# Performance work log

Hardware: AMD Instinct MI355X
Metric: run time of the kernel (lower is better)

Reference implementation:

```python
import jax, jax.numpy as jnp
import numpy as np

# Model dims
B, T, D = 1, 2048, 2048          # batch, seq_len, d_model
HI, DI = 4, 64                   # indexer heads / dim
H, DH = 16, 128                  # attention heads / head dim (H*DH == D)
TOPK = 512                       # sparse top-k tokens per query
NEG = -1e9


def setup_inputs() -> dict:
    key = jax.random.key(0)
    ks = jax.random.split(key, 8)
    s = 0.02  # weight init scale
    return {
        "hidden_states": jax.random.normal(ks[0], (B, T, D), jnp.float32),
        "Wq_idx": jax.random.normal(ks[1], (D, HI * DI), jnp.float32) * s,
        "Wk_idx": jax.random.normal(ks[2], (D, DI), jnp.float32) * s,
        "Ww_idx": jax.random.normal(ks[3], (D, HI), jnp.float32) * s,
        "Wq": jax.random.normal(ks[4], (D, H * DH), jnp.float32) * s,
        "Wk": jax.random.normal(ks[5], (D, H * DH), jnp.float32) * s,
        "Wv": jax.random.normal(ks[6], (D, H * DH), jnp.float32) * s,
        "Wo": jax.random.normal(ks[7], (H * DH, D), jnp.float32) * s,
    }


def reference(hidden_states, Wq_idx, Wk_idx, Ww_idx, Wq, Wk, Wv, Wo):
    x = hidden_states
    # ---- Lightning indexer: I[t,s] = sum_j w[t,j] * relu(q[t,j] . k[s]) ----
    qi = (x @ Wq_idx).reshape(B, T, HI, DI)          # [B,T,HI,DI]
    ki = x @ Wk_idx                                   # [B,S,DI]
    w = x @ Ww_idx                                    # [B,T,HI]
    dots = jnp.einsum('bthd,bsd->bths', qi, ki)       # [B,T,HI,S]
    index_scores = (jax.nn.relu(dots) * w[..., None]).sum(axis=2)  # [B,T,S]

    # ---- Top-k token selection with causal mask ----
    causal = jnp.triu(jnp.ones((T, T), dtype=bool), 1)            # True above diag
    masked_scores = jnp.where(causal[None], NEG, index_scores)
    _, top_idx = jax.lax.top_k(masked_scores, TOPK)               # [B,T,TOPK]
    b_ix = jnp.arange(B)[:, None, None]
    t_ix = jnp.arange(T)[None, :, None]
    top_mask = jnp.zeros((B, T, T), dtype=bool).at[b_ix, t_ix, top_idx].set(True)
    add_mask = jnp.where(top_mask, 0.0, NEG).astype(x.dtype)      # [B,T,S]

    # ---- Dense multi-head attention with additive sparse mask ----
    q = (x @ Wq).reshape(B, T, H, DH)
    k = (x @ Wk).reshape(B, T, H, DH)
    v = (x @ Wv).reshape(B, T, H, DH)
    scores = jnp.einsum('bthd,bshd->bhts', q, k) / np.sqrt(DH).astype(np.float32)
    scores = scores + add_mask[:, None]                            # [B,H,T,S]
    probs = jax.nn.softmax(scores, axis=-1)
    attn = jnp.einsum('bhts,bshd->bthd', probs, v).reshape(B, T, H * DH)
    attn_output = attn @ Wo                                        # [B,T,D]
    return attn_output
```

## Files before the change

kernel.cpp:

```cpp
#include <hip/hip_runtime.h>
#include <cstdint>
#include <cstddef>

#define T_DIM 2048
#define D_DIM 2048
#define HI_N 4
#define DI_N 64
#define H_N 16
#define DH_N 128
#define TOPK_N 512
#define NEG_F (-1e9f)
#define FA_NEG (-1e30f)

typedef __attribute__((ext_vector_type(8))) short short8;
typedef __attribute__((ext_vector_type(4))) float f32x4;
typedef unsigned short ushort_t;

__device__ __forceinline__ unsigned short f2bf(float f) {
  unsigned u = __float_as_uint(f);
  u += 0x7FFFu + ((u >> 16) & 1u);
  return (unsigned short)(u >> 16);
}
__device__ __forceinline__ float bf2f(unsigned short b) {
  return __uint_as_float((unsigned)b << 16);
}

#define GLDS(g, l) __builtin_amdgcn_global_load_lds( \
    (const __attribute__((address_space(1))) unsigned int*)(g), \
    (__attribute__((address_space(3))) unsigned int*)(l), 16, 0, 0)

#define IDXP_QI_F   524288
#define IDXP_KI_F   131072
#define IDXP_WI_F   8192
#define IDXP_STRIDE (IDXP_QI_F + IDXP_KI_F + IDXP_WI_F)

__global__ __launch_bounds__(256) void idx_proj(const float* __restrict__ x,
                                                const float* __restrict__ Wq_idx,
                                                const float* __restrict__ Wk_idx,
                                                const float* __restrict__ Ww_idx,
                                                float* __restrict__ parts) {
  __shared__ float As[2][16][64];
  __shared__ float Bs[2][16][64];
  const int bm = blockIdx.y << 6;
  const int bn_id = blockIdx.x;
  const int kbeg = blockIdx.z << 9;
  const int kend = kbeg + 512;
  float* part = parts + (size_t)blockIdx.z * IDXP_STRIDE;
  const float* B; float* C; int ldB, cb, ncols;
  if (bn_id < 4)       { B = Wq_idx; C = part;             ldB = 256; cb = bn_id << 6; ncols = 64; }
  else if (bn_id == 4) { B = Wk_idx; C = part + IDXP_QI_F; ldB = 64;  cb = 0;          ncols = 64; }
  else                 { B = Ww_idx; C = part + IDXP_QI_F + IDXP_KI_F; ldB = 4; cb = 0; ncols = 4; }
  const int tid = threadIdx.x;
  const int tx = tid & 15, ty = tid >> 4;
  const int am = tid >> 2;
  const int ak = (tid & 3) << 2;
  float acc[4][4] = {};

  float4 a4 = *(const float4*)&x[(size_t)(bm + am) * 2048 + kbeg + ak];
  float4 b4 = make_float4(0, 0, 0, 0);
  if ((tx << 2) < ncols) b4 = *(const float4*)&B[(size_t)(kbeg + ty) * ldB + cb + (tx << 2)];
  As[0][ak + 0][am] = a4.x; As[0][ak + 1][am] = a4.y;
  As[0][ak + 2][am] = a4.z; As[0][ak + 3][am] = a4.w;
  *(float4*)&Bs[0][ty][tx << 2] = b4;

  int p = 0;
  for (int k0 = kbeg; k0 < kend; k0 += 16) {
    __syncthreads();
    const bool more = (k0 + 16) < kend;
    if (more) {
      a4 = *(const float4*)&x[(size_t)(bm + am) * 2048 + k0 + 16 + ak];
      if ((tx << 2) < ncols)
        b4 = *(const float4*)&B[(size_t)(k0 + 16 + ty) * ldB + cb + (tx << 2)];
    }
#pragma unroll
    for (int kk = 0; kk < 16; ++kk) {
      float4 av4 = *(const float4*)&As[p][kk][ty << 2];
      float4 bv4 = *(const float4*)&Bs[p][kk][tx << 2];
      float av[4] = {av4.x, av4.y, av4.z, av4.w};
      float bv[4] = {bv4.x, bv4.y, bv4.z, bv4.w};
#pragma unroll
      for (int i = 0; i < 4; ++i)
#pragma unroll
        for (int j = 0; j < 4; ++j) acc[i][j] += av[i] * bv[j];
    }
    if (more) {
      As[1 - p][ak + 0][am] = a4.x; As[1 - p][ak + 1][am] = a4.y;
      As[1 - p][ak + 2][am] = a4.z; As[1 - p][ak + 3][am] = a4.w;
      *(float4*)&Bs[1 - p][ty][tx << 2] = b4;
    }
    p ^= 1;
  }
#pragma unroll
  for (int i = 0; i < 4; ++i) {
    int m = bm + (ty << 2) + i;
    int n0 = tx << 2;
    if (n0 + 3 < ncols) {
      *(float4*)&C[(size_t)m * ldB + cb + n0] =
          make_float4(acc[i][0], acc[i][1], acc[i][2], acc[i][3]);
    } else {
#pragma unroll
      for (int j = 0; j < 4; ++j)
        if (n0 + j < ncols) C[(size_t)m * ldB + cb + n0 + j] = acc[i][j];
    }
  }
}

__global__ __launch_bounds__(256) void idx_reduce(const float* __restrict__ parts,
                                                  float* __restrict__ qi,
                                                  float* __restrict__ ki,
                                                  float* __restrict__ wI) {
  const size_t f = ((size_t)blockIdx.x * 256 + threadIdx.x) * 4;
  float4 r0 = *(const float4*)(parts + f);
  float4 r1 = *(const float4*)(parts + (size_t)IDXP_STRIDE + f);
  float4 r2 = *(const float4*)(parts + (size_t)2 * IDXP_STRIDE + f);
  float4 r3 = *(const float4*)(parts + (size_t)3 * IDXP_STRIDE + f);
  float4 r;
  r.x = ((r0.x + r1.x) + r2.x) + r3.x;
  r.y = ((r0.y + r1.y) + r2.y) + r3.y;
  r.z = ((r0.z + r1.z) + r2.z) + r3.z;
  r.w = ((r0.w + r1.w) + r2.w) + r3.w;
  float* dst;
  if (f < IDXP_QI_F)                     dst = qi + f;
  else if (f < IDXP_QI_F + IDXP_KI_F)    dst = ki + (f - IDXP_QI_F);
  else                                   dst = wI + (f - IDXP_QI_F - IDXP_KI_F);
  *(float4*)dst = r;
}

__global__ __launch_bounds__(256) void cast_bf16(const float* __restrict__ in,
                                                 ushort_t* __restrict__ out) {
  int i = (blockIdx.x * 256 + threadIdx.x) * 4;
  float4 f = *(const float4*)(in + i);
  ushort4 o;
  o.x = f2bf(f.x); o.y = f2bf(f.y); o.z = f2bf(f.z); o.w = f2bf(f.w);
  *(ushort4*)(out + i) = o;
}

__global__ __launch_bounds__(256) void cast_transpose(const float* __restrict__ in,
                                                      ushort_t* __restrict__ out,
                                                      int R, int C) {
  __shared__ float tile[32][33];
  const int bx = blockIdx.x * 32;
  const int by = blockIdx.y * 32;
  const int tx = threadIdx.x & 31, ty = threadIdx.x >> 5;
#pragma unroll
  for (int i = 0; i < 32; i += 8)
    tile[ty + i][tx] = in[(size_t)(by + ty + i) * C + bx + tx];
  __syncthreads();
#pragma unroll
  for (int i = 0; i < 32; i += 8)
    out[(size_t)(bx + ty + i) * R + by + tx] = f2bf(tile[tx][ty + i]);
}

__global__ __launch_bounds__(256) void transpose_bf(const ushort_t* __restrict__ in,
                                                    ushort_t* __restrict__ out,
                                                    int ldin) {
  __shared__ ushort_t tile[64][68];
  const int bx = blockIdx.x * 64;
  const int by = blockIdx.y * 64;
  const int tid = threadIdx.x;
#pragma unroll
  for (int p = 0; p < 4; ++p) {
    int r = p * 16 + (tid >> 4), c0 = (tid & 15) * 4;
    *(ushort4*)&tile[r][c0] = *(const ushort4*)(in + (size_t)(by + r) * ldin + bx + c0);
  }
  __syncthreads();
#pragma unroll
  for (int p = 0; p < 4; ++p) {
    int r = p * 16 + (tid >> 4), c0 = (tid & 15) * 4;
    ushort4 o;
    o.x = tile[c0 + 0][r]; o.y = tile[c0 + 1][r];
    o.z = tile[c0 + 2][r]; o.w = tile[c0 + 3][r];
    *(ushort4*)(out + (size_t)(bx + r) * T_DIM + by + c0) = o;
  }
}

template <int OUT_BF16>
__global__ __launch_bounds__(256) void gemm_bt(const ushort_t* __restrict__ A,
                                               const ushort_t* __restrict__ Bt,
                                               void* __restrict__ C,
                                               int M, int N, int K) {
  __shared__ __attribute__((aligned(16))) ushort_t As[128 * 64];
  __shared__ __attribute__((aligned(16))) ushort_t Bs[128 * 64];
  const int bm = blockIdx.y << 7;
  const int bn = blockIdx.x << 7;
  const int tid = threadIdx.x;
  const int lane = tid & 63;
  const int wv = tid >> 6;
  const int wm = (wv >> 1) << 6;
  const int wn = (wv & 1) << 6;

  f32x4 acc[4][4] = {};

  const int sr = tid >> 3;
  const int sc = (tid & 7) << 3;
  const ushort_t* ga = A + (size_t)(bm + sr) * K + sc;
  const ushort_t* gb = Bt + (size_t)(bn + sr) * K + sc;
  const size_t rstep = (size_t)32 * K;

  for (int k0 = 0; k0 < K; k0 += 64) {
#pragma unroll
    for (int i = 0; i < 4; ++i) {
      GLDS(ga + i * rstep + k0, As + i * 2048 + tid * 8);
      GLDS(gb + i * rstep + k0, Bs + i * 2048 + tid * 8);
    }
    __syncthreads();
#pragma unroll
    for (int ks = 0; ks < 2; ++ks) {
      short8 af[4], bfr[4];
      const int kk = (ks << 5) + ((lane >> 4) << 3);
#pragma unroll
      for (int i = 0; i < 4; ++i) {
        af[i]  = *(const short8*)(As + (wm + (i << 4) + (lane & 15)) * 64 + kk);
        bfr[i] = *(const short8*)(Bs + (wn + (i << 4) + (lane & 15)) * 64 + kk);
      }
#pragma unroll
      for (int i = 0; i < 4; ++i)
#pragma unroll
        for (int j = 0; j < 4; ++j)
          acc[i][j] = __builtin_amdgcn_mfma_f32_16x16x32_bf16(af[i], bfr[j], acc[i][j], 0, 0, 0);
    }
    __syncthreads();
  }

  const int lrow = (lane >> 4) << 2;
  const int lcol = lane & 15;
#pragma unroll
  for (int i = 0; i < 4; ++i) {
    const int row = bm + wm + (i << 4) + lrow;
#pragma unroll
    for (int j = 0; j < 4; ++j) {
      const int col = bn + wn + (j << 4) + lcol;
#pragma unroll
      for (int r = 0; r < 4; ++r) {
        if (OUT_BF16)
          ((ushort_t*)C)[(size_t)(row + r) * N + col] = f2bf(acc[i][j][r]);
        else
          ((float*)C)[(size_t)(row + r) * N + col] = acc[i][j][r];
      }
    }
  }
}

__global__ __launch_bounds__(512, 2) void gemm256_bt(const ushort_t* __restrict__ A,
                                                     const ushort_t* __restrict__ Bt,
                                                     ushort_t* __restrict__ C,
                                                     int M, int N, int K) {
  __shared__ __attribute__((aligned(16))) ushort_t Ab[2][256 * 64];
  __shared__ __attribute__((aligned(16))) ushort_t Bb[2][256 * 64];
  const int bm = blockIdx.y << 8;
  const int bn = blockIdx.x << 8;
  const int tid = threadIdx.x;
  const int lane = tid & 63;
  const int wid = tid >> 6;
  const int wr = wid >> 2;
  const int wc = wid & 3;
  const int l15 = lane & 15, l4 = lane >> 4;
  const int srow = tid >> 3;
  const int schunk = tid & 7;
  const int swc = (schunk ^ (srow & 7)) << 3;
  const int NT = K >> 6;

  f32x4 acc[8][4] = {};

#define STAGE_A(b, h, kt) { \
    const ushort_t* g_ = A + (size_t)(bm + (h) * 64 + srow) * K + (kt) * 64 + swc; \
    GLDS(g_, Ab[b] + ((h) * 64 + srow) * 64 + (schunk << 3)); \
    GLDS(g_ + (size_t)128 * K, Ab[b] + (128 + (h) * 64 + srow) * 64 + (schunk << 3)); }

#define STAGE_B(b, h, kt) { \
    const int br_ = ((srow >= 32) ? 64 : 0) + (h) * 32 + (srow & 31); \
    const ushort_t* g_ = Bt + (size_t)(bn + br_) * K + (kt) * 64 + swc; \
    GLDS(g_, Bb[b] + br_ * 64 + (schunk << 3)); \
    GLDS(g_ + (size_t)128 * K, Bb[b] + (128 + br_) * 64 + (schunk << 3)); }

#define VMW(n) asm volatile("s_waitcnt vmcnt(" #n ")" ::: "memory")

#define PHASE(b, qm, qn, STG, WT) { \
    short8 paf[4][2], pbf[2][2]; \
    _Pragma("unroll") for (int m_ = 0; m_ < 4; ++m_) { \
      const int Ra_ = wr * 128 + (qm) * 64 + m_ * 16 + l15; \
      _Pragma("unroll") for (int ks_ = 0; ks_ < 2; ++ks_) \
        paf[m_][ks_] = *(const short8*)(Ab[b] + Ra_ * 64 + ((((ks_ << 2) + l4) ^ (Ra_ & 7)) << 3)); } \
    _Pragma("unroll") for (int n_ = 0; n_ < 2; ++n_) { \
      const int Rb_ = wc * 64 + (qn) * 32 + n_ * 16 + l15; \
      _Pragma("unroll") for (int ks_ = 0; ks_ < 2; ++ks_) \
        pbf[n_][ks_] = *(const short8*)(Bb[b] + Rb_ * 64 + ((((ks_ << 2) + l4) ^ (Rb_ & 7)) << 3)); } \
    STG; \
    WT; \
    asm volatile("" ::: "memory"); \
    __builtin_amdgcn_s_barrier(); \
    asm volatile("s_waitcnt lgkmcnt(0)" ::: "memory"); \
    __builtin_amdgcn_sched_barrier(0); \
    __builtin_amdgcn_s_setprio(1); \
    _Pragma("unroll") for (int m_ = 0; m_ < 4; ++m_) \
      _Pragma("unroll") for (int n_ = 0; n_ < 2; ++n_) \
        _Pragma("unroll") for (int ks_ = 0; ks_ < 2; ++ks_) \
          acc[(qm) * 4 + m_][(qn) * 2 + n_] = __builtin_amdgcn_mfma_f32_16x16x32_bf16( \
              paf[m_][ks_], pbf[n_][ks_], acc[(qm) * 4 + m_][(qn) * 2 + n_], 0, 0, 0); \
    __builtin_amdgcn_s_setprio(0); \
    asm volatile("" ::: "memory"); \
    __builtin_amdgcn_s_barrier(); \
    asm volatile("" ::: "memory"); }

  STAGE_A(0, 0, 0); STAGE_B(0, 0, 0); STAGE_A(0, 1, 0); STAGE_B(0, 1, 0);
  STAGE_A(1, 0, 1); STAGE_B(1, 0, 1);
  VMW(8);
  asm volatile("" ::: "memory");
  __builtin_amdgcn_s_barrier();
  asm volatile("" ::: "memory");

  for (int j = 0; j < NT / 2 - 1; ++j) {
    const int t = j * 2;
    PHASE(0, 0, 0, STAGE_A(1, 1, t + 1), VMW(6));
    PHASE(0, 0, 1, STAGE_B(1, 1, t + 1), );
    PHASE(0, 1, 0, STAGE_A(0, 0, t + 2), );
    PHASE(0, 1, 1, STAGE_B(0, 0, t + 2), VMW(8));
    PHASE(1, 0, 0, STAGE_A(0, 1, t + 2), VMW(6));
    PHASE(1, 0, 1, STAGE_B(0, 1, t + 2), );
    PHASE(1, 1, 0, STAGE_A(1, 0, t + 3), );
    PHASE(1, 1, 1, STAGE_B(1, 0, t + 3), VMW(8));
  }
  PHASE(0, 0, 0, STAGE_A(1, 1, NT - 1), VMW(6));
  PHASE(0, 0, 1, STAGE_B(1, 1, NT - 1), );
  PHASE(0, 1, 0, , );
  PHASE(0, 1, 1, , VMW(4));
  PHASE(1, 0, 0, , VMW(0));
  PHASE(1, 0, 1, , );
  PHASE(1, 1, 0, , );
  PHASE(1, 1, 1, , );

#undef STAGE_A
#undef STAGE_B
#undef VMW
#undef PHASE

#pragma unroll
  for (int i = 0; i < 8; ++i) {
    const int row = bm + wr * 128 + i * 16 + l4 * 4;
#pragma unroll
    for (int j2 = 0; j2 < 4; ++j2) {
      const int col = bn + wc * 64 + j2 * 16 + l15;
#pragma unroll
      for (int r = 0; r < 4; ++r)
        C[(size_t)(row + r) * N + col] = f2bf(acc[i][j2][r]);
    }
  }
}

__global__ __launch_bounds__(256) void idx_scores_rt(const float* __restrict__ qi,
                                                     const float* __restrict__ ki,
                                                     const float* __restrict__ w,
                                                     float* __restrict__ out) {
  const int t0 = blockIdx.y << 6, s0 = blockIdx.x << 6;
  const int tid = threadIdx.x;
  const int tx = tid & 15, ty = tid >> 4;
  if (s0 > t0 + 63) {
    const float4 nf = make_float4(NEG_F, NEG_F, NEG_F, NEG_F);
#pragma unroll
    for (int i = 0; i < 4; ++i) {
      int m = t0 + (ty << 2) + i;
      *(float4*)&out[(size_t)m * T_DIM + s0 + (tx << 2)] = nf;
    }
    return;
  }
  __shared__ float As[16][64];
  __shared__ float Bs[16][64];
  __shared__ float wsh[64][4];
  if (tid < 64) *(float4*)wsh[tid] = *(const float4*)&w[(size_t)(t0 + tid) * 4];
  const int am = tid >> 2;
  const int ak = (tid & 3) << 2;
  float oacc[4][4] = {};
#pragma unroll
  for (int h = 0; h < HI_N; ++h) {
    float dacc[4][4] = {};
    for (int k0 = 0; k0 < DI_N; k0 += 16) {
      float4 qa = *(const float4*)&qi[(size_t)(t0 + am) * 256 + h * DI_N + k0 + ak];
      float4 kb = *(const float4*)&ki[(size_t)(s0 + am) * DI_N + k0 + ak];
      __syncthreads();
      As[ak + 0][am] = qa.x; As[ak + 1][am] = qa.y;
      As[ak + 2][am] = qa.z; As[ak + 3][am] = qa.w;
      Bs[ak + 0][am] = kb.x; Bs[ak + 1][am] = kb.y;
      Bs[ak + 2][am] = kb.z; Bs[ak + 3][am] = kb.w;
      __syncthreads();
#pragma unroll
      for (int kk = 0; kk < 16; ++kk) {
        float4 a4 = *(const float4*)&As[kk][ty << 2];
        float4 b4 = *(const float4*)&Bs[kk][tx << 2];
        float av[4] = {a4.x, a4.y, a4.z, a4.w};
        float bv[4] = {b4.x, b4.y, b4.z, b4.w};
#pragma unroll
        for (int i = 0; i < 4; ++i)
#pragma unroll
          for (int j = 0; j < 4; ++j) dacc[i][j] += av[i] * bv[j];
      }
    }
#pragma unroll
    for (int i = 0; i < 4; ++i) {
      float wh = wsh[(ty << 2) + i][h];
#pragma unroll
      for (int j = 0; j < 4; ++j) oacc[i][j] += fmaxf(dacc[i][j], 0.f) * wh;
    }
  }
#pragma unroll
  for (int i = 0; i < 4; ++i) {
    int m = t0 + (ty << 2) + i;
    int n0 = s0 + (tx << 2);
    float4 r;
    r.x = (n0 + 0 > m) ? NEG_F : oacc[i][0];
    r.y = (n0 + 1 > m) ? NEG_F : oacc[i][1];
    r.z = (n0 + 2 > m) ? NEG_F : oacc[i][2];
    r.w = (n0 + 3 > m) ? NEG_F : oacc[i][3];
    *(float4*)&out[(size_t)m * T_DIM + n0] = r;
  }
}

__global__ __launch_bounds__(256) void select_mask(const float* __restrict__ scores,
                                                   unsigned long long* __restrict__ maskbits) {
  const int t = blockIdx.x, tid = threadIdx.x;
  __shared__ unsigned int hist[256];
  __shared__ unsigned int s_prefix, s_krem;
  __shared__ unsigned char bytes[256];
  unsigned int uv[8];
  const float* row = scores + (size_t)t * T_DIM;
  {
    float4 f0 = *(const float4*)(row + tid * 8);
    float4 f1 = *(const float4*)(row + tid * 8 + 4);
    float fv[8] = {f0.x, f0.y, f0.z, f0.w, f1.x, f1.y, f1.z, f1.w};
#pragma unroll
    for (int j = 0; j < 8; ++j) {
      unsigned u = __float_as_uint(fv[j]);
      uv[j] = (u & 0x80000000u) ? ~u : (u | 0x80000000u);
    }
  }
  if (tid == 0) { s_prefix = 0u; s_krem = TOPK_N; }
  for (int p = 0; p < 4; ++p) {
    const int sh = 24 - 8 * p;
    hist[tid] = 0;
    __syncthreads();
    const unsigned pm = p ? (0xFFFFFFFFu << (32 - 8 * p)) : 0u;
    const unsigned prefix = s_prefix;
#pragma unroll
    for (int j = 0; j < 8; ++j)
      if ((uv[j] & pm) == prefix) atomicAdd(&hist[(uv[j] >> sh) & 255], 1u);
    __syncthreads();
    if (tid == 0) {
      unsigned krem = s_krem, cum = 0;
      int b = 255;
      for (;; --b) { cum += hist[b]; if (cum >= krem) break; }
      s_prefix = prefix | ((unsigned)b << sh);
      s_krem = krem - (cum - hist[b]);
    }
    __syncthreads();
  }
  const unsigned V = s_prefix;
  const int kr = (int)s_krem;
  int eqc = 0;
#pragma unroll
  for (int j = 0; j < 8; ++j) eqc += (uv[j] == V);
  __syncthreads();
  hist[tid] = (unsigned)eqc;
  __syncthreads();
  for (int off = 1; off < 256; off <<= 1) {
    int v = (int)hist[tid];
    if (tid >= off) v += (int)hist[tid - off];
    __syncthreads();
    hist[tid] = (unsigned)v;
    __syncthreads();
  }
  int run = (int)hist[tid] - eqc;
  unsigned char byte = 0;
#pragma unroll
  for (int j = 0; j < 8; ++j) {
    bool eq = (uv[j] == V);
    bool take = (uv[j] > V) || (eq && run < kr);
    run += eq;
    byte |= (unsigned char)(take ? (1u << j) : 0u);
  }
  bytes[tid] = byte;
  __syncthreads();
  if (tid < 32) {
    unsigned long long wqw = 0;
#pragma unroll
    for (int b = 0; b < 8; ++b)
      wqw |= (unsigned long long)bytes[tid * 8 + b] << (8 * b);
    maskbits[(size_t)t * 32 + tid] = wqw;
  }
}

__global__ __launch_bounds__(256, 1) void flash_attn(
    const ushort_t* __restrict__ q, const ushort_t* __restrict__ k,
    const ushort_t* __restrict__ vt, const unsigned long long* __restrict__ maskbits,
    ushort_t* __restrict__ attn, int ldqk) {
  __shared__ __attribute__((aligned(16))) ushort_t Ks[2][128 * 128];
  __shared__ __attribute__((aligned(16))) ushort_t Vts[128 * 128];
  __shared__ __attribute__((aligned(16))) ushort_t Ps[128 * 136];

  const int tt = blockIdx.x;
  const int h  = blockIdx.y;
  const int t0 = tt << 7;
  const int tid = threadIdx.x;
  const int lane = tid & 63;
  const int wv = tid >> 6;
  const int l15 = lane & 15, l4 = lane >> 4;
  const int e3 = l15 & 7;
  const int scol = (((tid & 15) ^ ((tid >> 4) & 7)) << 3);

  {
    const ushort_t* gq = q + (size_t)(t0 + (tid >> 4)) * ldqk + h * DH_N + scol;
#pragma unroll
    for (int p = 0; p < 8; ++p)
      GLDS(gq + (size_t)p * 16 * ldqk, Ks[0] + p * 2048 + tid * 8);
  }
  asm volatile("s_waitcnt vmcnt(0)" ::: "memory");
  __builtin_amdgcn_s_barrier();
  asm volatile("" ::: "memory");
  short8 qfrag[4][2];
#pragma unroll
  for (int ks = 0; ks < 4; ++ks)
#pragma unroll
    for (int j = 0; j < 2; ++j)
      qfrag[ks][j] = *(const short8*)(Ks[0] + (wv * 32 + j * 16 + l15) * 128 +
                                      ((((ks << 2) + l4) ^ e3) << 3));
  asm volatile("s_waitcnt lgkmcnt(0)" ::: "memory");
  __builtin_amdgcn_s_barrier();
  asm volatile("" ::: "memory");

  f32x4 acc[8][2] = {};
  float m_reg[2] = {-INFINITY, -INFINITY};
  float l_reg[2] = {0.f, 0.f};
  const int nst = (tt < 4) ? 4 : (tt + 1);
  const float rsc = 0.08838834764831845f;

  {
    const ushort_t* gk = k + (size_t)(tid >> 4) * ldqk + h * DH_N + scol;
#pragma unroll
    for (int p = 0; p < 8; ++p)
      GLDS(gk + (size_t)p * 16 * ldqk, Ks[0] + p * 2048 + tid * 8);
  }

  for (int st = 0; st < nst; ++st) {
    const int s0 = st << 7;
    const bool pf = (st + 1) < nst;

    asm volatile("" ::: "memory");
    __builtin_amdgcn_s_barrier();
    asm volatile("" ::: "memory");

    unsigned long long mw[2][2];
    {
      const int wbase = s0 >> 6;
#pragma unroll
      for (int j = 0; j < 2; ++j)
#pragma unroll
        for (int wd = 0; wd < 2; ++wd)
          mw[j][wd] = maskbits[(size_t)(t0 + wv * 32 + j * 16 + l15) * 32 + wbase + wd];
    }
    {
      const ushort_t* gv = vt + (size_t)(h * DH_N + (tid >> 4)) * T_DIM + s0 + scol;
#pragma unroll
      for (int p = 0; p < 8; ++p)
        GLDS(gv + (size_t)p * 16 * T_DIM, Vts + p * 2048 + tid * 8);
    }
    asm volatile("" ::: "memory");
    if (pf) {
      const ushort_t* gk = k + (size_t)(s0 + 128 + (tid >> 4)) * ldqk + h * DH_N + scol;
      ushort_t* dst = Ks[(st + 1) & 1];
#pragma unroll
      for (int p = 0; p < 8; ++p)
        GLDS(gk + (size_t)p * 16 * ldqk, dst + p * 2048 + tid * 8);
    }
    if (pf) asm volatile("s_waitcnt vmcnt(20)" ::: "memory");
    else    asm volatile("s_waitcnt vmcnt(12)" ::: "memory");
    __builtin_amdgcn_s_barrier();
    asm volatile("" ::: "memory");

    const ushort_t* Kb = Ks[st & 1];
    f32x4 sacc[8][2] = {};
    __builtin_amdgcn_s_setprio(1);
#pragma unroll
    for (int ks = 0; ks < 4; ++ks) {
      const int co = ((((ks << 2) + l4) ^ e3) << 3);
      short8 af[8];
#pragma unroll
      for (int i = 0; i < 8; ++i)
        af[i] = *(const short8*)(Kb + (i * 16 + l15) * 128 + co);
#pragma unroll
      for (int i = 0; i < 8; ++i)
#pragma unroll
        for (int j = 0; j < 2; ++j)
          sacc[i][j] = __builtin_amdgcn_mfma_f32_16x16x32_bf16(af[i], qfrag[ks][j], sacc[i][j], 0, 0, 0);
    }
    __builtin_amdgcn_s_setprio(0);

#pragma unroll
    for (int i = 0; i < 8; ++i)
#pragma unroll
      for (int j = 0; j < 2; ++j)
#pragma unroll
        for (int r = 0; r < 4; ++r) {
          bool sel = (mw[j][i >> 2] >> ((i & 3) * 16 + l4 * 4 + r)) & 1;
          sacc[i][j][r] = sel ? sacc[i][j][r] * rsc : FA_NEG;
        }

    float alpha[2];
#pragma unroll
    for (int j = 0; j < 2; ++j) {
      float pm = sacc[0][j][0];
#pragma unroll
      for (int i = 0; i < 8; ++i)
#pragma unroll
        for (int r = 0; r < 4; ++r) pm = fmaxf(pm, sacc[i][j][r]);
      pm = fmaxf(pm, __shfl_xor(pm, 16));
      pm = fmaxf(pm, __shfl_xor(pm, 32));
      const float mn = fmaxf(m_reg[j], pm);
      alpha[j] = __expf(m_reg[j] - mn);
      float ps = 0.f;
#pragma unroll
      for (int i = 0; i < 8; ++i)
#pragma unroll
        for (int r = 0; r < 4; ++r) {
          float s = sacc[i][j][r];
          float pv = (s <= -1e29f) ? 0.f : __expf(s - mn);
          sacc[i][j][r] = pv;
          ps += pv;
        }
      ps += __shfl_xor(ps, 16);
      ps += __shfl_xor(ps, 32);
      l_reg[j] = alpha[j] * l_reg[j] + ps;
      m_reg[j] = mn;
    }
#pragma unroll
    for (int i = 0; i < 8; ++i)
#pragma unroll
      for (int j = 0; j < 2; ++j)
#pragma unroll
        for (int r = 0; r < 4; ++r) acc[i][j][r] *= alpha[j];

#pragma unroll
    for (int j = 0; j < 2; ++j)
#pragma unroll
      for (int i = 0; i < 8; ++i) {
        ushort4 pk;
        pk.x = f2bf(sacc[i][j][0]); pk.y = f2bf(sacc[i][j][1]);
        pk.z = f2bf(sacc[i][j][2]); pk.w = f2bf(sacc[i][j][3]);
        *(ushort4*)&Ps[(wv * 32 + j * 16 + l15) * 136 + i * 16 + l4 * 4] = pk;
      }

    if (pf) asm volatile("s_waitcnt vmcnt(8)" ::: "memory");
    else    asm volatile("s_waitcnt vmcnt(0)" ::: "memory");
    __builtin_amdgcn_s_barrier();
    asm volatile("" ::: "memory");

    __builtin_amdgcn_s_setprio(1);
#pragma unroll
    for (int ks = 0; ks < 4; ++ks) {
      const int co = ((((ks << 2) + l4) ^ e3) << 3);
      short8 af[8], bq[2];
#pragma unroll
      for (int i = 0; i < 8; ++i)
        af[i] = *(const short8*)(Vts + (i * 16 + l15) * 128 + co);
#pragma unroll
      for (int j = 0; j < 2; ++j)
        bq[j] = *(const short8*)(Ps + (wv * 32 + j * 16 + l15) * 136 + ks * 32 + l4 * 8);
#pragma unroll
      for (int i = 0; i < 8; ++i)
#pragma unroll
        for (int j = 0; j < 2; ++j)
          acc[i][j] = __builtin_amdgcn_mfma_f32_16x16x32_bf16(af[i], bq[j], acc[i][j], 0, 0, 0);
    }
    __builtin_amdgcn_s_setprio(0);
  }

  float linv[2];
#pragma unroll
  for (int j = 0; j < 2; ++j) linv[j] = 1.f / l_reg[j];
#pragma unroll
  for (int j = 0; j < 2; ++j)
#pragma unroll
    for (int i = 0; i < 8; ++i) {
      ushort4 pk;
      pk.x = f2bf(acc[i][j][0] * linv[j]);
      pk.y = f2bf(acc[i][j][1] * linv[j]);
      pk.z = f2bf(acc[i][j][2] * linv[j]);
      pk.w = f2bf(acc[i][j][3] * linv[j]);
      *(ushort4*)&Ps[(wv * 32 + j * 16 + l15) * 136 + i * 16 + l4 * 4] = pk;
    }
  __syncthreads();
#pragma unroll
  for (int p = 0; p < 8; ++p) {
    int rw = p * 16 + (tid >> 4);
    int d0 = (tid & 15) * 8;
    *(ulonglong2*)(attn + (size_t)(t0 + rw) * D_DIM + h * DH_N + d0) =
        *(const ulonglong2*)(Ps + rw * 136 + d0);
  }
}

extern "C" void kernel_launch(void* const* d_in, const int* in_sizes, int n_in,
                              void* d_out, int out_size, void* d_ws, size_t ws_size,
                              hipStream_t stream) {
  (void)in_sizes; (void)n_in; (void)out_size; (void)ws_size;
  const float* x      = (const float*)d_in[0];
  const float* Wq_idx = (const float*)d_in[1];
  const float* Wk_idx = (const float*)d_in[2];
  const float* Ww_idx = (const float*)d_in[3];
  const float* Wq     = (const float*)d_in[4];
  const float* Wk     = (const float*)d_in[5];
  const float* Wv     = (const float*)d_in[6];
  const float* Wo     = (const float*)d_in[7];
  float* out = (float*)d_out;

  char* ws = (char*)d_ws;
  const size_t MB = 1ull << 20;
  float*    parts   = (float*)(ws);
  float*    scores  = (float*)(ws);
  ushort_t* qkv_bf  = (ushort_t*)(ws);
  unsigned long long* maskbits = (unsigned long long*)(ws + 25 * MB + 512 * 1024);
  ushort_t* x_bf    = (ushort_t*)(ws + 26 * MB);
  ushort_t* Wcat_t  = (ushort_t*)(ws + 34 * MB);
  ushort_t* vt_bf   = (ushort_t*)(ws + 34 * MB);
  ushort_t* attn_bf = (ushort_t*)(ws + 42 * MB);
  ushort_t* Wo_t    = (ushort_t*)(ws + 58 * MB);
  float*    qi      = (float*)(ws + 66 * MB);
  float*    ki      = (float*)(ws + 68 * MB);
  float*    wI      = (float*)(ws + 68 * MB + 512 * 1024);

  const dim3 blk(256);
  const dim3 tgrid(D_DIM / 32, D_DIM / 32);

  cast_bf16<<<dim3((D_DIM * T_DIM) / 1024), blk, 0, stream>>>(x, x_bf);
  cast_transpose<<<tgrid, blk, 0, stream>>>(Wq, Wcat_t, D_DIM, D_DIM);
  cast_transpose<<<tgrid, blk, 0, stream>>>(Wk, Wcat_t + (size_t)D_DIM * D_DIM, D_DIM, D_DIM);
  cast_transpose<<<tgrid, blk, 0, stream>>>(Wv, Wcat_t + (size_t)2 * D_DIM * D_DIM, D_DIM, D_DIM);
  cast_transpose<<<tgrid, blk, 0, stream>>>(Wo, Wo_t, D_DIM, D_DIM);

  idx_proj<<<dim3(6, T_DIM / 64, 4), blk, 0, stream>>>(x, Wq_idx, Wk_idx, Ww_idx, parts);
  idx_reduce<<<dim3(IDXP_STRIDE / 1024), blk, 0, stream>>>(parts, qi, ki, wI);
  idx_scores_rt<<<dim3(T_DIM / 64, T_DIM / 64), blk, 0, stream>>>(qi, ki, wI, scores);
  select_mask<<<dim3(T_DIM), blk, 0, stream>>>(scores, maskbits);

  gemm256_bt<<<dim3(3 * D_DIM / 256, T_DIM / 256), dim3(512), 0, stream>>>(
      x_bf, Wcat_t, qkv_bf, T_DIM, 3 * D_DIM, D_DIM);

  transpose_bf<<<dim3(D_DIM / 64, T_DIM / 64), blk, 0, stream>>>(
      qkv_bf + 2 * D_DIM, vt_bf, 3 * D_DIM);

  flash_attn<<<dim3(T_DIM / 128, H_N), blk, 0, stream>>>(
      qkv_bf, qkv_bf + D_DIM, vt_bf, maskbits, attn_bf, 3 * D_DIM);

  gemm_bt<0><<<dim3(D_DIM / 128, T_DIM / 128), blk, 0, stream>>>(
      attn_bf, Wo_t, out, T_DIM, D_DIM, D_DIM);
}
```

Baseline: 494.0 us.

## Use 8 waves per flash-attention block with 16 query rows each

```diff
diff --git a/kernel.cpp b/kernel.cpp
--- a/kernel.cpp
+++ b/kernel.cpp
@@ -487,7 +487,7 @@
   }
 }
 
-__global__ __launch_bounds__(256, 1) void flash_attn(
+__global__ __launch_bounds__(512, 2) void flash_attn(
     const ushort_t* __restrict__ q, const ushort_t* __restrict__ k,
     const ushort_t* __restrict__ vt, const unsigned long long* __restrict__ maskbits,
     ushort_t* __restrict__ attn, int ldqk) {
@@ -508,34 +508,32 @@
   {
     const ushort_t* gq = q + (size_t)(t0 + (tid >> 4)) * ldqk + h * DH_N + scol;
 #pragma unroll
-    for (int p = 0; p < 8; ++p)
-      GLDS(gq + (size_t)p * 16 * ldqk, Ks[0] + p * 2048 + tid * 8);
+    for (int p = 0; p < 4; ++p)
+      GLDS(gq + (size_t)p * 32 * ldqk, Ks[0] + p * 4096 + tid * 8);
   }
   asm volatile("s_waitcnt vmcnt(0)" ::: "memory");
   __builtin_amdgcn_s_barrier();
   asm volatile("" ::: "memory");
-  short8 qfrag[4][2];
+  short8 qfrag[4];
 #pragma unroll
   for (int ks = 0; ks < 4; ++ks)
-#pragma unroll
-    for (int j = 0; j < 2; ++j)
-      qfrag[ks][j] = *(const short8*)(Ks[0] + (wv * 32 + j * 16 + l15) * 128 +
-                                      ((((ks << 2) + l4) ^ e3) << 3));
+    qfrag[ks] = *(const short8*)(Ks[0] + (wv * 16 + l15) * 128 +
+                                 ((((ks << 2) + l4) ^ e3) << 3));
   asm volatile("s_waitcnt lgkmcnt(0)" ::: "memory");
   __builtin_amdgcn_s_barrier();
   asm volatile("" ::: "memory");
 
-  f32x4 acc[8][2] = {};
-  float m_reg[2] = {-INFINITY, -INFINITY};
-  float l_reg[2] = {0.f, 0.f};
+  f32x4 acc[8] = {};
+  float m_reg = -INFINITY;
+  float l_reg = 0.f;
   const int nst = (tt < 4) ? 4 : (tt + 1);
   const float rsc = 0.08838834764831845f;
 
   {
     const ushort_t* gk = k + (size_t)(tid >> 4) * ldqk + h * DH_N + scol;
 #pragma unroll
-    for (int p = 0; p < 8; ++p)
-      GLDS(gk + (size_t)p * 16 * ldqk, Ks[0] + p * 2048 + tid * 8);
+    for (int p = 0; p < 4; ++p)
+      GLDS(gk + (size_t)p * 32 * ldqk, Ks[0] + p * 4096 + tid * 8);
   }
 
   for (int st = 0; st < nst; ++st) {
@@ -546,36 +544,34 @@
     __builtin_amdgcn_s_barrier();
     asm volatile("" ::: "memory");
 
-    unsigned long long mw[2][2];
+    unsigned long long mw[2];
     {
       const int wbase = s0 >> 6;
 #pragma unroll
-      for (int j = 0; j < 2; ++j)
-#pragma unroll
-        for (int wd = 0; wd < 2; ++wd)
-          mw[j][wd] = maskbits[(size_t)(t0 + wv * 32 + j * 16 + l15) * 32 + wbase + wd];
+      for (int wd = 0; wd < 2; ++wd)
+        mw[wd] = maskbits[(size_t)(t0 + wv * 16 + l15) * 32 + wbase + wd];
     }
     {
       const ushort_t* gv = vt + (size_t)(h * DH_N + (tid >> 4)) * T_DIM + s0 + scol;
 #pragma unroll
-      for (int p = 0; p < 8; ++p)
-        GLDS(gv + (size_t)p * 16 * T_DIM, Vts + p * 2048 + tid * 8);
+      for (int p = 0; p < 4; ++p)
+        GLDS(gv + (size_t)p * 32 * T_DIM, Vts + p * 4096 + tid * 8);
     }
     asm volatile("" ::: "memory");
     if (pf) {
       const ushort_t* gk = k + (size_t)(s0 + 128 + (tid >> 4)) * ldqk + h * DH_N + scol;
       ushort_t* dst = Ks[(st + 1) & 1];
 #pragma unroll
-      for (int p = 0; p < 8; ++p)
-        GLDS(gk + (size_t)p * 16 * ldqk, dst + p * 2048 + tid * 8);
-    }
-    if (pf) asm volatile("s_waitcnt vmcnt(20)" ::: "memory");
-    else    asm volatile("s_waitcnt vmcnt(12)" ::: "memory");
+      for (int p = 0; p < 4; ++p)
+        GLDS(gk + (size_t)p * 32 * ldqk, dst + p * 4096 + tid * 8);
+    }
+    if (pf) asm volatile("s_waitcnt vmcnt(10)" ::: "memory");
+    else    asm volatile("s_waitcnt vmcnt(6)" ::: "memory");
     __builtin_amdgcn_s_barrier();
     asm volatile("" ::: "memory");
 
     const ushort_t* Kb = Ks[st & 1];
-    f32x4 sacc[8][2] = {};
+    f32x4 sacc[8] = {};
     __builtin_amdgcn_s_setprio(1);
 #pragma unroll
     for (int ks = 0; ks < 4; ++ks) {
@@ -586,67 +582,58 @@
         af[i] = *(const short8*)(Kb + (i * 16 + l15) * 128 + co);
 #pragma unroll
       for (int i = 0; i < 8; ++i)
-#pragma unroll
-        for (int j = 0; j < 2; ++j)
-          sacc[i][j] = __builtin_amdgcn_mfma_f32_16x16x32_bf16(af[i], qfrag[ks][j], sacc[i][j], 0, 0, 0);
+        sacc[i] = __builtin_amdgcn_mfma_f32_16x16x32_bf16(af[i], qfrag[ks], sacc[i], 0, 0, 0);
     }
     __builtin_amdgcn_s_setprio(0);
 
 #pragma unroll
     for (int i = 0; i < 8; ++i)
 #pragma unroll
-      for (int j = 0; j < 2; ++j)
-#pragma unroll
-        for (int r = 0; r < 4; ++r) {
-          bool sel = (mw[j][i >> 2] >> ((i & 3) * 16 + l4 * 4 + r)) & 1;
-          sacc[i][j][r] = sel ? sacc[i][j][r] * rsc : FA_NEG;
-        }
-
-    float alpha[2];
-#pragma unroll
-    for (int j = 0; j < 2; ++j) {
-      float pm = sacc[0][j][0];
+      for (int r = 0; r < 4; ++r) {
+        bool sel = (mw[i >> 2] >> ((i & 3) * 16 + l4 * 4 + r)) & 1;
+        sacc[i][r] = sel ? sacc[i][r] * rsc : FA_NEG;
+      }
+
+    float alpha;
+    {
+      float pm = sacc[0][0];
 #pragma unroll
       for (int i = 0; i < 8; ++i)
 #pragma unroll
-        for (int r = 0; r < 4; ++r) pm = fmaxf(pm, sacc[i][j][r]);
+        for (int r = 0; r < 4; ++r) pm = fmaxf(pm, sacc[i][r]);
       pm = fmaxf(pm, __shfl_xor(pm, 16));
       pm = fmaxf(pm, __shfl_xor(pm, 32));
-      const float mn = fmaxf(m_reg[j], pm);
-      alpha[j] = __expf(m_reg[j] - mn);
+      const float mn = fmaxf(m_reg, pm);
+      alpha = __expf(m_reg - mn);
       float ps = 0.f;
 #pragma unroll
       for (int i = 0; i < 8; ++i)
 #pragma unroll
         for (int r = 0; r < 4; ++r) {
-          float s = sacc[i][j][r];
+          float s = sacc[i][r];
           float pv = (s <= -1e29f) ? 0.f : __expf(s - mn);
-          sacc[i][j][r] = pv;
+          sacc[i][r] = pv;
           ps += pv;
         }
       ps += __shfl_xor(ps, 16);
       ps += __shfl_xor(ps, 32);
-      l_reg[j] = alpha[j] * l_reg[j] + ps;
-      m_reg[j] = mn;
+      l_reg = alpha * l_reg + ps;
+      m_reg = mn;
     }
 #pragma unroll
     for (int i = 0; i < 8; ++i)
 #pragma unroll
-      for (int j = 0; j < 2; ++j)
-#pragma unroll
-        for (int r = 0; r < 4; ++r) acc[i][j][r] *= alpha[j];
-
-#pragma unroll
-    for (int j = 0; j < 2; ++j)
-#pragma unroll
-      for (int i = 0; i < 8; ++i) {
-        ushort4 pk;
-        pk.x = f2bf(sacc[i][j][0]); pk.y = f2bf(sacc[i][j][1]);
-        pk.z = f2bf(sacc[i][j][2]); pk.w = f2bf(sacc[i][j][3]);
-        *(ushort4*)&Ps[(wv * 32 + j * 16 + l15) * 136 + i * 16 + l4 * 4] = pk;
-      }
-
-    if (pf) asm volatile("s_waitcnt vmcnt(8)" ::: "memory");
+      for (int r = 0; r < 4; ++r) acc[i][r] *= alpha;
+
+#pragma unroll
+    for (int i = 0; i < 8; ++i) {
+      ushort4 pk;
+      pk.x = f2bf(sacc[i][0]); pk.y = f2bf(sacc[i][1]);
+      pk.z = f2bf(sacc[i][2]); pk.w = f2bf(sacc[i][3]);
+      *(ushort4*)&Ps[(wv * 16 + l15) * 136 + i * 16 + l4 * 4] = pk;
+    }
+
+    if (pf) asm volatile("s_waitcnt vmcnt(4)" ::: "memory");
     else    asm volatile("s_waitcnt vmcnt(0)" ::: "memory");
     __builtin_amdgcn_s_barrier();
     asm volatile("" ::: "memory");
@@ -655,40 +642,32 @@
 #pragma unroll
     for (int ks = 0; ks < 4; ++ks) {
       const int co = ((((ks << 2) + l4) ^ e3) << 3);
-      short8 af[8], bq[2];
+      short8 af[8], bq;
 #pragma unroll
       for (int i = 0; i < 8; ++i)
         af[i] = *(const short8*)(Vts + (i * 16 + l15) * 128 + co);
-#pragma unroll
-      for (int j = 0; j < 2; ++j)
-        bq[j] = *(const short8*)(Ps + (wv * 32 + j * 16 + l15) * 136 + ks * 32 + l4 * 8);
+      bq = *(const short8*)(Ps + (wv * 16 + l15) * 136 + ks * 32 + l4 * 8);
 #pragma unroll
       for (int i = 0; i < 8; ++i)
-#pragma unroll
-        for (int j = 0; j < 2; ++j)
-          acc[i][j] = __builtin_amdgcn_mfma_f32_16x16x32_bf16(af[i], bq[j], acc[i][j], 0, 0, 0);
+        acc[i] = __builtin_amdgcn_mfma_f32_16x16x32_bf16(af[i], bq, acc[i], 0, 0, 0);
     }
     __builtin_amdgcn_s_setprio(0);
   }
 
-  float linv[2];
-#pragma unroll
-  for (int j = 0; j < 2; ++j) linv[j] = 1.f / l_reg[j];
-#pragma unroll
-  for (int j = 0; j < 2; ++j)
-#pragma unroll
-    for (int i = 0; i < 8; ++i) {
-      ushort4 pk;
-      pk.x = f2bf(acc[i][j][0] * linv[j]);
-      pk.y = f2bf(acc[i][j][1] * linv[j]);
-      pk.z = f2bf(acc[i][j][2] * linv[j]);
-      pk.w = f2bf(acc[i][j][3] * linv[j]);
-      *(ushort4*)&Ps[(wv * 32 + j * 16 + l15) * 136 + i * 16 + l4 * 4] = pk;
-    }
+  const float linv = 1.f / l_reg;
+#pragma unroll
+  for (int i = 0; i < 8; ++i) {
+    ushort4 pk;
+    pk.x = f2bf(acc[i][0] * linv);
+    pk.y = f2bf(acc[i][1] * linv);
+    pk.z = f2bf(acc[i][2] * linv);
+    pk.w = f2bf(acc[i][3] * linv);
+    *(ushort4*)&Ps[(wv * 16 + l15) * 136 + i * 16 + l4 * 4] = pk;
+  }
   __syncthreads();
 #pragma unroll
-  for (int p = 0; p < 8; ++p) {
-    int rw = p * 16 + (tid >> 4);
+  for (int p = 0; p < 4; ++p) {
+    int rw = p * 32 + (tid >> 4);
     int d0 = (tid & 15) * 8;
     *(ulonglong2*)(attn + (size_t)(t0 + rw) * D_DIM + h * DH_N + d0) =
         *(const ulonglong2*)(Ps + rw * 136 + d0);
@@ -744,7 +723,7 @@
   transpose_bf<<<dim3(D_DIM / 64, T_DIM / 64), blk, 0, stream>>>(
       qkv_bf + 2 * D_DIM, vt_bf, 3 * D_DIM);
 
-  flash_attn<<<dim3(T_DIM / 128, H_N), blk, 0, stream>>>(
+  flash_attn<<<dim3(T_DIM / 128, H_N), dim3(512), 0, stream>>>(
       qkv_bf, qkv_bf + D_DIM, vt_bf, maskbits, attn_bf, 3 * D_DIM);
 
   gemm_bt<0><<<dim3(D_DIM / 128, T_DIM / 128), blk, 0, stream>>>(
```

Result: no change. 485.3 us (-1.7%).
